# Performance work log

Measured on AMD Instinct MI355X. Metric: run time of the kernel, lower is better.

## Reference

```python
import jax, jax.numpy as jnp
import numpy as np

B, C, N = 4, 32, 256
D_IN, D_EMB, K = 512, 1024, 4096  # input_dim, llm_embedding_dim, codebook_size
EPS = 1e-12


def setup_inputs() -> dict:
    key = jax.random.key(0)
    ks = jax.random.split(key, 6)
    s_in = float(1.0 / np.sqrt(D_IN))
    s_emb = float(1.0 / np.sqrt(D_EMB))
    return {
        "x": jax.random.normal(ks[0], (B, C, N, D_IN), jnp.float32),
        # nn.Linear(input_dim, llm_embedding_dim): weight [out, in], uniform(-1/sqrt(in), 1/sqrt(in))
        "w_in": jax.random.uniform(ks[1], (D_EMB, D_IN), jnp.float32, -s_in, s_in),
        "b_in": jax.random.uniform(ks[2], (D_EMB,), jnp.float32, -s_in, s_in),
        "w_out": jax.random.uniform(ks[3], (D_IN, D_EMB), jnp.float32, -s_emb, s_emb),
        "b_out": jax.random.uniform(ks[4], (D_IN,), jnp.float32, -s_emb, s_emb),
        # frozen LLM-embedding codebook (copied from llm_embedding_bank, requires_grad=False)
        "codebook": jax.random.normal(ks[5], (K, D_EMB), jnp.float32),
    }


def _rotate_to(src, tgt):
    # Rotation trick (arXiv:2410.06424, sec 4.2) as in vector-quantize-pytorch.
    # Forward value equals tgt; gradient flows through src via a (detached)
    # Householder rotation + scaling.
    n_src = jnp.linalg.norm(src, axis=-1, keepdims=True)
    n_tgt = jnp.linalg.norm(tgt, axis=-1, keepdims=True)
    u = jax.lax.stop_gradient(src / jnp.maximum(n_src, EPS))   # unit src, detached
    q = tgt / jnp.maximum(n_tgt, EPS)                          # unit tgt (codebook: no grad)
    w = u + q
    w = jax.lax.stop_gradient(w / jnp.maximum(jnp.linalg.norm(w, axis=-1, keepdims=True), EPS))
    rot = (src
           - 2.0 * jnp.sum(src * w, -1, keepdims=True) * w
           + 2.0 * jnp.sum(src * u, -1, keepdims=True) * q)
    return rot * jax.lax.stop_gradient(n_tgt / jnp.maximum(n_src, EPS))


def reference(x, w_in, b_in, w_out, b_out, codebook):
    Bb, Cc, Nn, _ = x.shape
    # input projection, flatten channels x patches into token axis
    z = jnp.einsum('bcnd,ed->bcne', x, w_in) + b_in          # [B, C, N, D_EMB]
    z = z.reshape(Bb, Cc * Nn, -1)                           # [B, T, D_EMB]
    # squared euclidean distances to codebook: ||z||^2 - 2 z.c + ||c||^2
    dists = (jnp.sum(z * z, -1, keepdims=True)
             - 2.0 * jnp.einsum('bte,ke->btk', z, codebook)
             + jnp.sum(codebook * codebook, -1))             # [B, T, K]
    indices = jnp.argmin(dists, axis=-1)                     # [B, T] int
    q = codebook[indices]                                    # gather [B, T, D_EMB]
    quantized = _rotate_to(z, q)                             # == q in value
    # commitment loss (commitment_weight = 1.0); codebook frozen -> only commit term
    aux_loss = jnp.mean((jax.lax.stop_gradient(quantized) - z) ** 2)
    out = jnp.einsum('bte,de->btd', quantized, w_out) + b_out
    return (out.reshape(Bb, Cc, Nn, -1),
            indices,
            quantized.reshape(Bb, Cc, Nn, -1),
            aux_loss)
```

## Files before the change

### kernel.cpp

```cpp
#include <hip/hip_runtime.h>

#define M_TOK 32768
#define DIN   512
#define DEMB  1024
#define KC    4096

#define IDX_OFF ((size_t)M_TOK * DIN)
#define Q_OFF   (IDX_OFF + M_TOK)
#define AUX_OFF (Q_OFF + (size_t)M_TOK * DEMB)

typedef _Float16 f16x8 __attribute__((ext_vector_type(8)));
typedef _Float16 f16x4 __attribute__((ext_vector_type(4)));
typedef float f32x4 __attribute__((ext_vector_type(4)));

__device__ inline void gload16(const void* g, void* s) {
    __builtin_amdgcn_global_load_lds((const __attribute__((address_space(1))) void*)g,
                                     (__attribute__((address_space(3))) void*)s, 16, 0, 0);
}

__device__ inline unsigned umin2(unsigned a, unsigned b) { return a < b ? a : b; }
__device__ inline unsigned umax2(unsigned a, unsigned b) { return a > b ? a : b; }

__device__ inline float block_reduce_sum_256(float v) {
#pragma unroll
    for (int off = 32; off > 0; off >>= 1) v += __shfl_down(v, off);
    __shared__ float smem[4];
    const int lane = threadIdx.x & 63;
    const int w = threadIdx.x >> 6;
    if (lane == 0) smem[w] = v;
    __syncthreads();
    return smem[0] + smem[1] + smem[2] + smem[3];
}

__global__ __launch_bounds__(256) void prep_all(const float* __restrict__ cb,
                                                const float* __restrict__ w_out,
                                                const float* __restrict__ w_in,
                                                _Float16* __restrict__ cbf,
                                                _Float16* __restrict__ wof,
                                                _Float16* __restrict__ wh,
                                                _Float16* __restrict__ wl,
                                                _Float16* __restrict__ cbp,
                                                float* __restrict__ cn2p,
                                                float* __restrict__ aux) {
    const int b = blockIdx.x;
    if (b < 4096) {
        if (b == 0 && threadIdx.x == 0) *aux = 0.0f;
        const float4 v = reinterpret_cast<const float4*>(cb + (size_t)b * DEMB)[threadIdx.x];
        f16x4 h;
        h[0] = (_Float16)v.x; h[1] = (_Float16)v.y; h[2] = (_Float16)v.z; h[3] = (_Float16)v.w;
        reinterpret_cast<f16x4*>(cbf + (size_t)b * DEMB)[threadIdx.x] = h;
        float s = v.x * v.x + v.y * v.y + v.z * v.z + v.w * v.w;
        s = block_reduce_sum_256(s);
        if (threadIdx.x == 0) cn2p[b] = 0.5f * s + 1024.0f;
    } else if (b < 4352) {
        const size_t i = (size_t)(b - 4096) * 256 + threadIdx.x;
        const float4 a = reinterpret_cast<const float4*>(w_out)[i * 2];
        const float4 b4 = reinterpret_cast<const float4*>(w_out)[i * 2 + 1];
        f16x8 h;
        h[0] = (_Float16)a.x; h[1] = (_Float16)a.y; h[2] = (_Float16)a.z; h[3] = (_Float16)a.w;
        h[4] = (_Float16)b4.x; h[5] = (_Float16)b4.y; h[6] = (_Float16)b4.z; h[7] = (_Float16)b4.w;
        reinterpret_cast<f16x8*>(wof)[i] = h;
    } else if (b < 4608) {
        const size_t i = (size_t)(b - 4352) * 256 + threadIdx.x;
        const float4 a = reinterpret_cast<const float4*>(w_in)[i * 2];
        const float4 b4 = reinterpret_cast<const float4*>(w_in)[i * 2 + 1];
        const float e[8] = {a.x, a.y, a.z, a.w, b4.x, b4.y, b4.z, b4.w};
        f16x8 h, l8;
#pragma unroll
        for (int j = 0; j < 8; ++j) {
            const _Float16 hv = (_Float16)e[j];
            h[j] = hv;
            l8[j] = (_Float16)((e[j] - (float)hv) * 2048.0f);
        }
        reinterpret_cast<f16x8*>(wh)[i] = h;
        reinterpret_cast<f16x8*>(wl)[i] = l8;
    } else {
        const int id = (b - 4608) * 256 + threadIdx.x;
        const int c16 = id >> 11;
        const int rem = id & 2047;
        const int kk = rem >> 6;
        const int l = rem & 63;
        const int lgq = l >> 4, lcq = l & 15;
        const float* src = cb + ((size_t)(c16 * 16 + lcq)) * DEMB + kk * 32 + lgq * 8;
        const float4 a = *reinterpret_cast<const float4*>(src);
        const float4 b4 = *reinterpret_cast<const float4*>(src + 4);
        f16x8 h;
        h[0] = (_Float16)a.x; h[1] = (_Float16)a.y; h[2] = (_Float16)a.z; h[3] = (_Float16)a.w;
        h[4] = (_Float16)b4.x; h[5] = (_Float16)b4.y; h[6] = (_Float16)b4.z; h[7] = (_Float16)b4.w;
        const int ntile = c16 >> 2, nn = c16 & 3;
        const size_t off = ((size_t)(kk * 256 + ntile * 4 + nn)) * 64 + l;
        *reinterpret_cast<f16x8*>(cbp + off * 8) = h;
    }
}

__global__ __launch_bounds__(256, 2) void zgemm_split(const float* __restrict__ x,
                                                      const _Float16* __restrict__ wh,
                                                      const _Float16* __restrict__ wl,
                                                      const float* __restrict__ bin,
                                                      float* __restrict__ zq,
                                                      _Float16* __restrict__ zf) {
    extern __shared__ char smem[];
    _Float16* Ah = (_Float16*)smem;
    _Float16* Al = Ah + 8192;
    _Float16* Bh = Al + 8192;
    _Float16* Bl = Bh + 8192;
    const int t = threadIdx.x;
    const int w = t >> 6, l = t & 63;
    const int wm = w >> 1, wn = w & 1;
    const int lg = l >> 4, lc = l & 15;
    const int m0 = blockIdx.y * 128, n0 = blockIdx.x * 128;

    const int ar = t >> 3;
    const int ach = t & 7;
    const int aswz = ach ^ (ar & 7);

    f32x4 acc1[4][4] = {};
    f32x4 acc2[4][4] = {};

    for (int kt = 0; kt < 8; ++kt) {
        __syncthreads();
#pragma unroll
        for (int i = 0; i < 4; ++i) {
            const int row = i * 32 + ar;
            const size_t goff = (size_t)(n0 + row) * DIN + kt * 64 + aswz * 8;
            gload16(wh + goff, Bh + (size_t)(i * 256 + t) * 8);
            gload16(wl + goff, Bl + (size_t)(i * 256 + t) * 8);
        }
#pragma unroll
        for (int i = 0; i < 4; ++i) {
            const int row = i * 32 + ar;
            const float* px = x + (size_t)(m0 + row) * DIN + kt * 64 + ach * 8;
            const float4 a = *reinterpret_cast<const float4*>(px);
            const float4 b = *reinterpret_cast<const float4*>(px + 4);
            const float e[8] = {a.x, a.y, a.z, a.w, b.x, b.y, b.z, b.w};
            f16x8 h, l8;
#pragma unroll
            for (int j = 0; j < 8; ++j) {
                const _Float16 hv = (_Float16)e[j];
                h[j] = hv;
                l8[j] = (_Float16)((e[j] - (float)hv) * 2048.0f);
            }
            const int slot = row * 8 + aswz;
            *reinterpret_cast<f16x8*>(Ah + (size_t)slot * 8) = h;
            *reinterpret_cast<f16x8*>(Al + (size_t)slot * 8) = l8;
        }
        __syncthreads();
#pragma unroll
        for (int kk = 0; kk < 2; ++kk) {
            f16x8 ah[4], al8[4], bh[4], bl8[4];
#pragma unroll
            for (int m = 0; m < 4; ++m) {
                const int r = wm * 64 + m * 16 + lc;
                const int c = (kk * 4 + lg) ^ (lc & 7);
                ah[m] = *reinterpret_cast<const f16x8*>(Ah + (size_t)(r * 8 + c) * 8);
                al8[m] = *reinterpret_cast<const f16x8*>(Al + (size_t)(r * 8 + c) * 8);
            }
#pragma unroll
            for (int n = 0; n < 4; ++n) {
                const int r = wn * 64 + n * 16 + lc;
                const int c = (kk * 4 + lg) ^ (lc & 7);
                bh[n] = *reinterpret_cast<const f16x8*>(Bh + (size_t)(r * 8 + c) * 8);
                bl8[n] = *reinterpret_cast<const f16x8*>(Bl + (size_t)(r * 8 + c) * 8);
            }
            __builtin_amdgcn_s_setprio(1);
#pragma unroll
            for (int m = 0; m < 4; ++m)
#pragma unroll
                for (int n = 0; n < 4; ++n) {
                    acc1[m][n] = __builtin_amdgcn_mfma_f32_16x16x32_f16(ah[m], bh[n], acc1[m][n], 0, 0, 0);
                    acc2[m][n] = __builtin_amdgcn_mfma_f32_16x16x32_f16(ah[m], bl8[n], acc2[m][n], 0, 0, 0);
                    acc2[m][n] = __builtin_amdgcn_mfma_f32_16x16x32_f16(al8[m], bh[n], acc2[m][n], 0, 0, 0);
                }
            __builtin_amdgcn_s_setprio(0);
        }
    }
#pragma unroll
    for (int n = 0; n < 4; ++n) {
        const int col = n0 + wn * 64 + n * 16 + lc;
        const float bb = bin[col];
#pragma unroll
        for (int m = 0; m < 4; ++m)
#pragma unroll
            for (int r = 0; r < 4; ++r) {
                const int row = m0 + wm * 64 + m * 16 + lg * 4 + r;
                const float z = acc1[m][n][r] + acc2[m][n][r] * (1.0f / 2048.0f) + bb;
                zq[(size_t)row * DEMB + col] = z;
                zf[(size_t)row * DEMB + col] = (_Float16)(-z);
            }
    }
}

__global__ void __launch_bounds__(512)
__attribute__((amdgpu_waves_per_eu(2, 2)))
dist_topk(const _Float16* __restrict__ zf,
          const _Float16* __restrict__ cbp,
          const float* __restrict__ cn2p,
          unsigned* __restrict__ pk) {
    extern __shared__ _Float16 zt[];
    const int t = threadIdx.x;
    const int w = t >> 6, l = t & 63;
    const int lg = l >> 4, lc = l & 15;
    const int m0 = blockIdx.x * 64;

    {
        const int r0 = t >> 7;
        const int ch = t & 127;
#pragma unroll
        for (int i = 0; i < 16; ++i) {
            const int row = i * 4 + r0;
            const int sch = (ch & 0x70) | ((ch ^ row) & 15);
            gload16(zf + (((size_t)(m0 + row)) << 10) + sch * 8,
                    zt + ((size_t)(i * 512 + t)) * 8);
        }
    }

    const char* ztb = (const char*)zt;
    int lbase[4][4];
#pragma unroll
    for (int m = 0; m < 4; ++m)
#pragma unroll
        for (int j = 0; j < 4; ++j)
            lbase[m][j] = (m * 16 + lc) * 2048 + ((((j * 4) | lg) ^ lc) << 4);

    unsigned k0[16], k1[16];
#pragma unroll
    for (int r = 0; r < 16; ++r) { k0[r] = 0xFFFFFFFFu; k1[r] = 0xFFFFFFFFu; }

    const char* pL = (const char*)cbp + l * 16;

    f16x8 bf[4][4];
    {
#pragma unroll
        for (int s = 0; s < 4; ++s)
#pragma unroll
            for (int n = 0; n < 4; ++n)
                bf[s][n] = *reinterpret_cast<const f16x8*>(pL + s * 262144 + w * 4096 + n * 1024);
    }
    __syncthreads();

    f16x8 af[4][4];
#pragma unroll
    for (int s = 0; s < 2; ++s)
#pragma unroll
        for (int m = 0; m < 4; ++m)
            af[s][m] = *reinterpret_cast<const f16x8*>(ztb + lbase[m][s] + ((s & 28) << 6));

    unsigned boff = (unsigned)(w * 4096 + 4 * 262144);
    for (int nt8 = 0; nt8 < 8; ++nt8) {
        const int ntile = nt8 * 8 + w;
        const unsigned wrapAdd = (unsigned)((nt8 < 7 ? 8 : -56) * 4096 - 31 * 262144);
        const int colb = ntile * 64;
        unsigned colw[4];
        float c2[4];
#pragma unroll
        for (int n = 0; n < 4; ++n) {
            colw[n] = (unsigned)(colb + n * 16 + lc);
            c2[n] = cn2p[colw[n]];
        }
        f32x4 acc[4][4];
#pragma unroll
        for (int m = 0; m < 4; ++m)
#pragma unroll
            for (int n = 0; n < 4; ++n)
                acc[m][n] = (f32x4){c2[n], c2[n], c2[n], c2[n]};

#pragma unroll
        for (int kk = 0; kk < 32; ++kk) {
            const int nk2 = (kk + 2) & 31;
#pragma unroll
            for (int m = 0; m < 4; ++m)
                af[(kk + 2) & 3][m] = *reinterpret_cast<const f16x8*>(
                    ztb + lbase[m][nk2 & 3] + ((nk2 & 28) << 6));
            __builtin_amdgcn_s_setprio(1);
#pragma unroll
            for (int m = 0; m < 4; ++m)
#pragma unroll
                for (int n = 0; n < 4; ++n)
                    acc[m][n] = __builtin_amdgcn_mfma_f32_16x16x32_f16(
                        af[kk & 3][m], bf[kk & 3][n], acc[m][n], 0, 0, 0);
            __builtin_amdgcn_s_setprio(0);
#pragma unroll
            for (int n = 0; n < 4; ++n)
                bf[kk & 3][n] = *reinterpret_cast<const f16x8*>(pL + boff + n * 1024);
            boff += (kk == 27) ? wrapAdd : 262144u;
        }

#pragma unroll
        for (int n = 0; n < 4; ++n) {
#pragma unroll
            for (int m = 0; m < 4; ++m)
#pragma unroll
                for (int rg = 0; rg < 4; ++rg) {
                    const unsigned key =
                        (__float_as_uint(acc[m][n][rg]) & 0xFFFFF000u) | colw[n];
                    const int r = m * 4 + rg;
                    const unsigned kmax = umax2(k0[r], key);
                    k0[r] = umin2(k0[r], key);
                    k1[r] = umin2(k1[r], kmax);
                }
        }
    }
#pragma unroll
    for (int off = 1; off < 16; off <<= 1) {
#pragma unroll
        for (int r = 0; r < 16; ++r) {
            const unsigned b0 = __shfl_xor(k0[r], off);
            const unsigned b1 = __shfl_xor(k1[r], off);
            const unsigned lo = umin2(k0[r], b0);
            const unsigned hi = umax2(k0[r], b0);
            k0[r] = lo;
            k1[r] = umin2(hi, umin2(k1[r], b1));
        }
    }
    if (lc == 0) {
#pragma unroll
        for (int m = 0; m < 4; ++m)
#pragma unroll
            for (int rg = 0; rg < 4; ++rg) {
                const int r = m * 4 + rg;
                const int tok = m0 + m * 16 + lg * 4 + rg;
                pk[(size_t)(w * 2 + 0) * M_TOK + tok] = k0[r];
                pk[(size_t)(w * 2 + 1) * M_TOK + tok] = k1[r];
            }
    }
}

__global__ __launch_bounds__(256) void refine_idx(const float* __restrict__ cb,
                                                  const float* __restrict__ cn2p,
                                                  const unsigned* __restrict__ pk,
                                                  float* __restrict__ zq,
                                                  float* __restrict__ idx_f,
                                                  int* __restrict__ idx_i,
                                                  float* __restrict__ aux) {
    const int wv = threadIdx.x >> 6;
    const int t = blockIdx.x * 4 + wv;
    const int l = threadIdx.x & 63;
    float4* zp = reinterpret_cast<float4*>(zq + ((size_t)t << 10));
    float4 zr[4];
#pragma unroll
    for (int j = 0; j < 4; ++j) zr[j] = zp[l + j * 64];

    float zn = 0.0f;
#pragma unroll
    for (int j = 0; j < 4; ++j) {
        zn = fmaf(zr[j].x, zr[j].x, zn);
        zn = fmaf(zr[j].y, zr[j].y, zn);
        zn = fmaf(zr[j].z, zr[j].z, zn);
        zn = fmaf(zr[j].w, zr[j].w, zn);
    }
#pragma unroll
    for (int off = 1; off < 64; off <<= 1) zn += __shfl_xor(zn, off);

    unsigned v = 0xFFFFFFFFu;
    if (l < 16) v = pk[(size_t)l * M_TOK + t];

    float bestd = 3.4e38f;
    int besti = 0x7fffffff;
#pragma unroll
    for (int s = 0; s < 4; ++s) {
        unsigned mv = v;
#pragma unroll
        for (int off = 1; off < 64; off <<= 1) mv = umin2(mv, __shfl_xor(mv, off));
        if (v == mv) v = 0xFFFFFFFFu;
        const int mi = (int)(mv & 0xFFFu);
        const float4* cp = reinterpret_cast<const float4*>(cb + ((size_t)mi << 10));
        float s4 = 0.0f;
#pragma unroll
        for (int j = 0; j < 4; ++j) {
            const float4 c = cp[l + j * 64];
            s4 = fmaf(zr[j].x, c.x, s4);
            s4 = fmaf(zr[j].y, c.y, s4);
            s4 = fmaf(zr[j].z, c.z, s4);
            s4 = fmaf(zr[j].w, c.w, s4);
        }
#pragma unroll
        for (int off = 1; off < 64; off <<= 1) s4 += __shfl_xor(s4, off);
        const float d = cn2p[mi] - s4;
        if (d < bestd || (d == bestd && mi < besti)) { bestd = d; besti = mi; }
    }
    const float4* cpb = reinterpret_cast<const float4*>(cb + ((size_t)besti << 10));
#pragma unroll
    for (int j = 0; j < 4; ++j) zp[l + j * 64] = cpb[l + j * 64];

    __shared__ float dsum[4];
    if (l == 0) {
        idx_f[t] = (float)besti;
        idx_i[t] = besti;
        dsum[wv] = 2.0f * bestd - 2048.0f + zn;
    }
    __syncthreads();
    if (threadIdx.x == 0)
        atomicAdd(aux, (dsum[0] + dsum[1] + dsum[2] + dsum[3]) * (1.0f / 33554432.0f));
}

__global__ __launch_bounds__(256, 2) void outgemm(const _Float16* __restrict__ cbf,
                                                  const _Float16* __restrict__ wof,
                                                  const float* __restrict__ bout,
                                                  const int* __restrict__ idx,
                                                  float* __restrict__ out) {
    extern __shared__ char smem[];
    _Float16* As = (_Float16*)smem;
    _Float16* Bs = As + 16384;
    const int t = threadIdx.x;
    const int w = t >> 6, l = t & 63;
    const int wm = w >> 1, wn = w & 1;
    const int lg = l >> 4, lc = l & 15;
    const int m0 = blockIdx.y * 128, n0 = blockIdx.x * 128;

    const int sr = t >> 4;
    const int sch = t & 15;
    const int sswz = sch ^ (sr & 15);

    int arow[8];
#pragma unroll
    for (int i = 0; i < 8; ++i) arow[i] = idx[m0 + i * 16 + sr];

    f32x4 acc[4][4] = {};
    for (int kt = 0; kt < 8; ++kt) {
        __syncthreads();
#pragma unroll
        for (int i = 0; i < 8; ++i) {
            gload16(cbf + (size_t)arow[i] * DEMB + kt * 128 + sswz * 8,
                    As + (size_t)(i * 256 + t) * 8);
            gload16(wof + (size_t)(n0 + i * 16 + sr) * DEMB + kt * 128 + sswz * 8,
                    Bs + (size_t)(i * 256 + t) * 8);
        }
        __syncthreads();
#pragma unroll
        for (int kk = 0; kk < 4; ++kk) {
            f16x8 af[4], bf8[4];
#pragma unroll
            for (int m = 0; m < 4; ++m) {
                const int r = wm * 64 + m * 16 + lc;
                const int c = (kk * 4 + lg) ^ lc;
                af[m] = *reinterpret_cast<const f16x8*>(As + (size_t)(r * 16 + c) * 8);
            }
#pragma unroll
            for (int n = 0; n < 4; ++n) {
                const int r = wn * 64 + n * 16 + lc;
                const int c = (kk * 4 + lg) ^ lc;
                bf8[n] = *reinterpret_cast<const f16x8*>(Bs + (size_t)(r * 16 + c) * 8);
            }
            __builtin_amdgcn_s_setprio(1);
#pragma unroll
            for (int m = 0; m < 4; ++m)
#pragma unroll
                for (int n = 0; n < 4; ++n)
                    acc[m][n] = __builtin_amdgcn_mfma_f32_16x16x32_f16(af[m], bf8[n], acc[m][n], 0, 0, 0);
            __builtin_amdgcn_s_setprio(0);
        }
    }
#pragma unroll
    for (int n = 0; n < 4; ++n) {
        const int col = n0 + wn * 64 + n * 16 + lc;
        const float bb = bout[col];
#pragma unroll
        for (int m = 0; m < 4; ++m)
#pragma unroll
            for (int r = 0; r < 4; ++r) {
                const int row = m0 + wm * 64 + m * 16 + lg * 4 + r;
                out[(size_t)row * DIN + col] = acc[m][n][r] + bb;
            }
    }
}

extern "C" void kernel_launch(void* const* d_in, const int* in_sizes, int n_in,
                              void* d_out, int out_size, void* d_ws, size_t ws_size,
                              hipStream_t stream) {
    const float* x = (const float*)d_in[0];
    const float* w_in = (const float*)d_in[1];
    const float* b_in = (const float*)d_in[2];
    const float* w_out = (const float*)d_in[3];
    const float* b_out = (const float*)d_in[4];
    const float* cb = (const float*)d_in[5];

    float* out = (float*)d_out;
    float* idx_f = out + IDX_OFF;
    float* zq = out + Q_OFF;
    float* aux = out + AUX_OFF;
    _Float16* zf = (_Float16*)d_out;

    char* ws = (char*)d_ws;
    float* cn2p = (float*)ws;
    int* idx_i = (int*)(ws + 16384);
    unsigned* pk = (unsigned*)(ws + 147456);
    _Float16* cbf = (_Float16*)(ws + 4341760);
    _Float16* cbp = (_Float16*)(ws + 12730368);
    _Float16* wh = (_Float16*)(ws + 21118976);
    _Float16* wl = (_Float16*)(ws + 22167552);
    _Float16* wof = (_Float16*)(ws + 23216128);

    prep_all<<<6656, 256, 0, stream>>>(cb, w_out, w_in, cbf, wof, wh, wl, cbp, cn2p, aux);
    zgemm_split<<<dim3(DEMB / 128, M_TOK / 128), 256, 65536, stream>>>(x, wh, wl, b_in, zq, zf);
    dist_topk<<<M_TOK / 64, 512, 131072, stream>>>(zf, cbp, cn2p, pk);
    refine_idx<<<M_TOK / 4, 256, 0, stream>>>(cb, cn2p, pk, zq, idx_f, idx_i, aux);
    outgemm<<<dim3(DIN / 128, M_TOK / 128), 256, 65536, stream>>>(cbf, wof, b_out, idx_i, out);
}
```

Before: 543.8 us.

## Restructure input projection to keep token tile resident and stream packed weights

Replaces the 128x128 tiled split-precision z-GEMM with a kernel in which each 512-thread block converts a 64-token slice of x to hi/lo fp16 once and keeps it in LDS. The block then streams the whole w_in, pre-packed by prep_all into the MFMA fragment layout, straight from global memory into registers with double buffering. This removes the repeated x conversion and the per-k-step LDS staging and barriers of the old kernel, and folds the bias into the accumulator initialisation. The cost is that every block rereads the full weight matrix from L2, and the kernel now uses 128KB of LDS with high register pressure.

```diff
diff --git a/kernel.cpp b/kernel.cpp
--- a/kernel.cpp
+++ b/kernel.cpp
@@ -37,8 +37,7 @@
                                                 const float* __restrict__ w_in,
                                                 _Float16* __restrict__ cbf,
                                                 _Float16* __restrict__ wof,
-                                                _Float16* __restrict__ wh,
-                                                _Float16* __restrict__ wl,
+                                                _Float16* __restrict__ wpk,
                                                 _Float16* __restrict__ cbp,
                                                 float* __restrict__ cn2p,
                                                 float* __restrict__ aux) {
@@ -60,22 +59,8 @@
         h[0] = (_Float16)a.x; h[1] = (_Float16)a.y; h[2] = (_Float16)a.z; h[3] = (_Float16)a.w;
         h[4] = (_Float16)b4.x; h[5] = (_Float16)b4.y; h[6] = (_Float16)b4.z; h[7] = (_Float16)b4.w;
         reinterpret_cast<f16x8*>(wof)[i] = h;
-    } else if (b < 4608) {
-        const size_t i = (size_t)(b - 4352) * 256 + threadIdx.x;
-        const float4 a = reinterpret_cast<const float4*>(w_in)[i * 2];
-        const float4 b4 = reinterpret_cast<const float4*>(w_in)[i * 2 + 1];
-        const float e[8] = {a.x, a.y, a.z, a.w, b4.x, b4.y, b4.z, b4.w};
-        f16x8 h, l8;
-#pragma unroll
-        for (int j = 0; j < 8; ++j) {
-            const _Float16 hv = (_Float16)e[j];
-            h[j] = hv;
-            l8[j] = (_Float16)((e[j] - (float)hv) * 2048.0f);
-        }
-        reinterpret_cast<f16x8*>(wh)[i] = h;
-        reinterpret_cast<f16x8*>(wl)[i] = l8;
-    } else {
-        const int id = (b - 4608) * 256 + threadIdx.x;
+    } else if (b < 6400) {
+        const int id = (b - 4352) * 256 + threadIdx.x;
         const int c16 = id >> 11;
         const int rem = id & 2047;
         const int kk = rem >> 6;
@@ -90,103 +75,150 @@
         const int ntile = c16 >> 2, nn = c16 & 3;
         const size_t off = ((size_t)(kk * 256 + ntile * 4 + nn)) * 64 + l;
         *reinterpret_cast<f16x8*>(cbp + off * 8) = h;
-    }
-}
-
-__global__ __launch_bounds__(256, 2) void zgemm_split(const float* __restrict__ x,
-                                                      const _Float16* __restrict__ wh,
-                                                      const _Float16* __restrict__ wl,
-                                                      const float* __restrict__ bin,
-                                                      float* __restrict__ zq,
-                                                      _Float16* __restrict__ zf) {
-    extern __shared__ char smem[];
-    _Float16* Ah = (_Float16*)smem;
-    _Float16* Al = Ah + 8192;
-    _Float16* Bh = Al + 8192;
-    _Float16* Bl = Bh + 8192;
+    } else {
+        const int id = (b - 6400) * 256 + threadIdx.x;
+        const int l = id & 63;
+        const int hl = (id >> 6) & 1;
+        const int c16 = (id >> 7) & 63;
+        const int kk = id >> 13;
+        const int col = c16 * 16 + (l & 15);
+        const int kb = kk * 32 + (l >> 4) * 8;
+        const float* src = w_in + (size_t)col * DIN + kb;
+        const float4 a = *reinterpret_cast<const float4*>(src);
+        const float4 b4 = *reinterpret_cast<const float4*>(src + 4);
+        const float e[8] = {a.x, a.y, a.z, a.w, b4.x, b4.y, b4.z, b4.w};
+        f16x8 o;
+#pragma unroll
+        for (int j = 0; j < 8; ++j) {
+            const _Float16 hv = (_Float16)e[j];
+            o[j] = hl ? (_Float16)((e[j] - (float)hv) * 2048.0f) : hv;
+        }
+        *reinterpret_cast<f16x8*>(wpk + (size_t)id * 8) = o;
+    }
+}
+
+__global__ void __launch_bounds__(512)
+__attribute__((amdgpu_waves_per_eu(2, 2)))
+zgemm_stream(const float* __restrict__ x,
+             const _Float16* __restrict__ wpk,
+             const float* __restrict__ bin,
+             float* __restrict__ zq,
+             _Float16* __restrict__ zf) {
+    extern __shared__ _Float16 sm[];
+    _Float16* Ah = sm;
+    _Float16* Al = sm + 32768;
     const int t = threadIdx.x;
     const int w = t >> 6, l = t & 63;
-    const int wm = w >> 1, wn = w & 1;
     const int lg = l >> 4, lc = l & 15;
-    const int m0 = blockIdx.y * 128, n0 = blockIdx.x * 128;
-
-    const int ar = t >> 3;
-    const int ach = t & 7;
-    const int aswz = ach ^ (ar & 7);
-
-    f32x4 acc1[4][4] = {};
-    f32x4 acc2[4][4] = {};
-
-    for (int kt = 0; kt < 8; ++kt) {
-        __syncthreads();
-#pragma unroll
-        for (int i = 0; i < 4; ++i) {
-            const int row = i * 32 + ar;
-            const size_t goff = (size_t)(n0 + row) * DIN + kt * 64 + aswz * 8;
-            gload16(wh + goff, Bh + (size_t)(i * 256 + t) * 8);
-            gload16(wl + goff, Bl + (size_t)(i * 256 + t) * 8);
-        }
-#pragma unroll
-        for (int i = 0; i < 4; ++i) {
-            const int row = i * 32 + ar;
-            const float* px = x + (size_t)(m0 + row) * DIN + kt * 64 + ach * 8;
+    const int m0 = blockIdx.x * 64;
+
+    {
+        const int r = t >> 3;
+        const int c0 = t & 7;
+#pragma unroll
+        for (int i = 0; i < 8; ++i) {
+            const int c = c0 + i * 8;
+            const float* px = x + (size_t)(m0 + r) * DIN + c * 8;
             const float4 a = *reinterpret_cast<const float4*>(px);
-            const float4 b = *reinterpret_cast<const float4*>(px + 4);
-            const float e[8] = {a.x, a.y, a.z, a.w, b.x, b.y, b.z, b.w};
-            f16x8 h, l8;
+            const float4 b4 = *reinterpret_cast<const float4*>(px + 4);
+            const float e[8] = {a.x, a.y, a.z, a.w, b4.x, b4.y, b4.z, b4.w};
+            f16x8 h, lo;
 #pragma unroll
             for (int j = 0; j < 8; ++j) {
                 const _Float16 hv = (_Float16)e[j];
                 h[j] = hv;
-                l8[j] = (_Float16)((e[j] - (float)hv) * 2048.0f);
-            }
-            const int slot = row * 8 + aswz;
-            *reinterpret_cast<f16x8*>(Ah + (size_t)slot * 8) = h;
-            *reinterpret_cast<f16x8*>(Al + (size_t)slot * 8) = l8;
-        }
-        __syncthreads();
-#pragma unroll
-        for (int kk = 0; kk < 2; ++kk) {
-            f16x8 ah[4], al8[4], bh[4], bl8[4];
+                lo[j] = (_Float16)((e[j] - (float)hv) * 2048.0f);
+            }
+            const int swz = (c & 0x30) | ((c ^ r) & 15);
+            *reinterpret_cast<f16x8*>(Ah + (size_t)(r * 64 + swz) * 8) = h;
+            *reinterpret_cast<f16x8*>(Al + (size_t)(r * 64 + swz) * 8) = lo;
+        }
+    }
+
+    const char* ztb = (const char*)sm;
+    int lbase[4][4];
+#pragma unroll
+    for (int m = 0; m < 4; ++m)
+#pragma unroll
+        for (int j = 0; j < 4; ++j)
+            lbase[m][j] = (m * 16 + lc) * 1024 + ((((j * 4) | lg) ^ lc) & 15) * 16;
+
+    const char* pL = (const char*)wpk + w * 4096 + l * 16;
+
+    f16x8 bh[2][2], bl[2][2];
+#pragma unroll
+    for (int s = 0; s < 2; ++s)
+#pragma unroll
+        for (int n = 0; n < 2; ++n) {
+            bh[s][n] = *reinterpret_cast<const f16x8*>(pL + s * 131072 + n * 2048);
+            bl[s][n] = *reinterpret_cast<const f16x8*>(pL + s * 131072 + n * 2048 + 1024);
+        }
+
+    __syncthreads();
+
+    f16x8 ah[2][4], al[2][4];
+#pragma unroll
+    for (int m = 0; m < 4; ++m) {
+        ah[0][m] = *reinterpret_cast<const f16x8*>(ztb + lbase[m][0]);
+        al[0][m] = *reinterpret_cast<const f16x8*>(ztb + 65536 + lbase[m][0]);
+    }
+
+    unsigned boff = 2u * 131072u;
+    for (int p = 0; p < 4; ++p) {
+        f32x4 acc1[4][2], acc2[4][2];
+#pragma unroll
+        for (int n = 0; n < 2; ++n) {
+            const float bb = bin[p * 256 + w * 32 + n * 16 + lc];
 #pragma unroll
             for (int m = 0; m < 4; ++m) {
-                const int r = wm * 64 + m * 16 + lc;
-                const int c = (kk * 4 + lg) ^ (lc & 7);
-                ah[m] = *reinterpret_cast<const f16x8*>(Ah + (size_t)(r * 8 + c) * 8);
-                al8[m] = *reinterpret_cast<const f16x8*>(Al + (size_t)(r * 8 + c) * 8);
-            }
-#pragma unroll
-            for (int n = 0; n < 4; ++n) {
-                const int r = wn * 64 + n * 16 + lc;
-                const int c = (kk * 4 + lg) ^ (lc & 7);
-                bh[n] = *reinterpret_cast<const f16x8*>(Bh + (size_t)(r * 8 + c) * 8);
-                bl8[n] = *reinterpret_cast<const f16x8*>(Bl + (size_t)(r * 8 + c) * 8);
+                acc1[m][n] = (f32x4){bb, bb, bb, bb};
+                acc2[m][n] = (f32x4){0.f, 0.f, 0.f, 0.f};
+            }
+        }
+        const unsigned wrapAdd = (unsigned)((p < 3 ? 1 : -3) * 32768 - 15 * 131072);
+#pragma unroll
+        for (int kk = 0; kk < 16; ++kk) {
+            const int nk = (kk + 1) & 15;
+#pragma unroll
+            for (int m = 0; m < 4; ++m) {
+                ah[(kk + 1) & 1][m] = *reinterpret_cast<const f16x8*>(
+                    ztb + lbase[m][nk & 3] + ((nk >> 2) << 8));
+                al[(kk + 1) & 1][m] = *reinterpret_cast<const f16x8*>(
+                    ztb + 65536 + lbase[m][nk & 3] + ((nk >> 2) << 8));
             }
             __builtin_amdgcn_s_setprio(1);
 #pragma unroll
             for (int m = 0; m < 4; ++m)
 #pragma unroll
-                for (int n = 0; n < 4; ++n) {
-                    acc1[m][n] = __builtin_amdgcn_mfma_f32_16x16x32_f16(ah[m], bh[n], acc1[m][n], 0, 0, 0);
-                    acc2[m][n] = __builtin_amdgcn_mfma_f32_16x16x32_f16(ah[m], bl8[n], acc2[m][n], 0, 0, 0);
-                    acc2[m][n] = __builtin_amdgcn_mfma_f32_16x16x32_f16(al8[m], bh[n], acc2[m][n], 0, 0, 0);
+                for (int n = 0; n < 2; ++n) {
+                    acc1[m][n] = __builtin_amdgcn_mfma_f32_16x16x32_f16(
+                        ah[kk & 1][m], bh[kk & 1][n], acc1[m][n], 0, 0, 0);
+                    acc2[m][n] = __builtin_amdgcn_mfma_f32_16x16x32_f16(
+                        ah[kk & 1][m], bl[kk & 1][n], acc2[m][n], 0, 0, 0);
+                    acc2[m][n] = __builtin_amdgcn_mfma_f32_16x16x32_f16(
+                        al[kk & 1][m], bh[kk & 1][n], acc2[m][n], 0, 0, 0);
                 }
             __builtin_amdgcn_s_setprio(0);
-        }
-    }
-#pragma unroll
-    for (int n = 0; n < 4; ++n) {
-        const int col = n0 + wn * 64 + n * 16 + lc;
-        const float bb = bin[col];
-#pragma unroll
-        for (int m = 0; m < 4; ++m)
-#pragma unroll
-            for (int r = 0; r < 4; ++r) {
-                const int row = m0 + wm * 64 + m * 16 + lg * 4 + r;
-                const float z = acc1[m][n][r] + acc2[m][n][r] * (1.0f / 2048.0f) + bb;
-                zq[(size_t)row * DEMB + col] = z;
-                zf[(size_t)row * DEMB + col] = (_Float16)(-z);
-            }
+#pragma unroll
+            for (int n = 0; n < 2; ++n) {
+                bh[kk & 1][n] = *reinterpret_cast<const f16x8*>(pL + boff + n * 2048);
+                bl[kk & 1][n] = *reinterpret_cast<const f16x8*>(pL + boff + n * 2048 + 1024);
+            }
+            boff += (kk == 13) ? wrapAdd : 131072u;
+        }
+#pragma unroll
+        for (int n = 0; n < 2; ++n) {
+            const int col = p * 256 + w * 32 + n * 16 + lc;
+#pragma unroll
+            for (int m = 0; m < 4; ++m)
+#pragma unroll
+                for (int rg = 0; rg < 4; ++rg) {
+                    const int row = m0 + m * 16 + lg * 4 + rg;
+                    const float z = acc1[m][n][rg] + acc2[m][n][rg] * (1.0f / 2048.0f);
+                    zq[(size_t)row * DEMB + col] = z;
+                    zf[(size_t)row * DEMB + col] = (_Float16)(-z);
+                }
+        }
     }
 }
 
@@ -486,12 +518,11 @@
     unsigned* pk = (unsigned*)(ws + 147456);
     _Float16* cbf = (_Float16*)(ws + 4341760);
     _Float16* cbp = (_Float16*)(ws + 12730368);
-    _Float16* wh = (_Float16*)(ws + 21118976);
-    _Float16* wl = (_Float16*)(ws + 22167552);
+    _Float16* wpk = (_Float16*)(ws + 21118976);
     _Float16* wof = (_Float16*)(ws + 23216128);
 
-    prep_all<<<6656, 256, 0, stream>>>(cb, w_out, w_in, cbf, wof, wh, wl, cbp, cn2p, aux);
-    zgemm_split<<<dim3(DEMB / 128, M_TOK / 128), 256, 65536, stream>>>(x, wh, wl, b_in, zq, zf);
+    prep_all<<<6912, 256, 0, stream>>>(cb, w_out, w_in, cbf, wof, wpk, cbp, cn2p, aux);
+    zgemm_stream<<<M_TOK / 64, 512, 131072, stream>>>(x, wpk, b_in, zq, zf);
     dist_topk<<<M_TOK / 64, 512, 131072, stream>>>(zf, cbp, cn2p, pk);
     refine_idx<<<M_TOK / 4, 256, 0, stream>>>(cb, cn2p, pk, zq, idx_f, idx_i, aux);
     outgemm<<<dim3(DIN / 128, M_TOK / 128), 256, 65536, stream>>>(cbf, wof, b_out, idx_i, out);
```

Result: faster. 515.4 us (-5.2%).
